# Kernel optimization log

Hardware: AMD Instinct MI355X
Metric: run time of the kernel (lower is better)

The kernel has to match this reference:

```python
import jax, jax.numpy as jnp
import numpy as np

B, N, H, STEPS, IN_DIM, OUT_DIM = 512, 81, 128, 16, 10, 9
LN_EPS = 1e-5


def _build_edges():
    # Sudoku constraint graph: edge (j -> i) if cells share row, col, or 3x3 box.
    edges = []
    for i in range(81):
        ri, ci = divmod(i, 9)
        bi = ri // 3 * 3 + ci // 3
        for j in range(81):
            if i == j:
                continue
            rj, cj = divmod(j, 9)
            bj = rj // 3 * 3 + cj // 3
            if ri == rj or ci == cj or bi == bj:
                edges.append((j, i))
    e = np.asarray(edges, dtype=np.int32).T  # [2, 1620]
    return e[0], e[1]


def setup_inputs() -> dict:
    key = jax.random.key(0)
    ks = jax.random.split(key, 24)
    s = 0.02

    def w(k, shape):
        return jax.random.normal(k, shape, dtype=jnp.float32) * s

    src_np, dst_np = _build_edges()
    inp = {
        "x": jax.random.normal(ks[0], (B, N, IN_DIM), dtype=jnp.float32),
        "src": jnp.asarray(src_np),
        "dst": jnp.asarray(dst_np),
        "W_in": w(ks[1], (IN_DIM, H)), "b_in": jnp.zeros((H,), jnp.float32),
        "pos": w(ks[2], (N, H)),
        # message MLP: (2H -> H -> H -> H -> H), ReLU between
        "mW0": w(ks[3], (2 * H, H)), "mb0": jnp.zeros((H,), jnp.float32),
        "mW1": w(ks[4], (H, H)), "mb1": jnp.zeros((H,), jnp.float32),
        "mW2": w(ks[5], (H, H)), "mb2": jnp.zeros((H,), jnp.float32),
        "mW3": w(ks[6], (H, H)), "mb3": jnp.zeros((H,), jnp.float32),
        # node MLP: (3H -> H -> H -> H -> H)
        "nW0": w(ks[7], (3 * H, H)), "nb0": jnp.zeros((H,), jnp.float32),
        "nW1": w(ks[8], (H, H)), "nb1": jnp.zeros((H,), jnp.float32),
        "nW2": w(ks[9], (H, H)), "nb2": jnp.zeros((H,), jnp.float32),
        "nW3": w(ks[10], (H, H)), "nb3": jnp.zeros((H,), jnp.float32),
        "ln_g": jnp.ones((H,), jnp.float32), "ln_b": jnp.zeros((H,), jnp.float32),
        "W_out": w(ks[11], (H, OUT_DIM)), "b_out": jnp.zeros((OUT_DIM,), jnp.float32),
    }
    return inp


def _mlp(x, Ws, bs):
    for W, b in zip(Ws[:-1], bs[:-1]):
        x = jax.nn.relu(x @ W + b)
    return x @ Ws[-1] + bs[-1]


def _layer_norm(h, g, b):
    mu = jnp.mean(h, axis=-1, keepdims=True)
    var = jnp.mean(jnp.square(h - mu), axis=-1, keepdims=True)
    return (h - mu) * jax.lax.rsqrt(var + LN_EPS) * g + b


def reference(x, src, dst, W_in, b_in, pos,
              mW0, mb0, mW1, mb1, mW2, mb2, mW3, mb3,
              nW0, nb0, nW1, nb1, nW2, nb2, nW3, nb3,
              ln_g, ln_b, W_out, b_out):
    mWs, mbs = [mW0, mW1, mW2, mW3], [mb0, mb1, mb2, mb3]
    nWs, nbs = [nW0, nW1, nW2, nW3], [nb0, nb1, nb2, nb3]

    x_embed = x @ W_in + b_in + pos  # [B, N, H]
    h = x_embed
    for _ in range(STEPS):
        h_src = h[:, src]  # [B, E, H] gather
        h_dst = h[:, dst]
        messages = _mlp(jnp.concatenate([h_src, h_dst], axis=-1), mWs, mbs)  # [B, E, H]
        # scatter-add over dst -> [B, N, H]
        aggregated = jnp.zeros_like(h).at[:, dst, :].add(messages)
        h = h + _mlp(jnp.concatenate([h, x_embed, aggregated], axis=-1), nWs, nbs)
        h = _layer_norm(h, ln_g, ln_b)
    return h @ W_out + b_out  # [B, N, 9]
```

## Files before the change

### kernel.cpp

```cpp
#include <hip/hip_runtime.h>
#include <hip/hip_bf16.h>

typedef __bf16 bf16_t;
typedef bf16_t bf16x8 __attribute__((ext_vector_type(8)));
typedef bf16_t bf16x4 __attribute__((ext_vector_type(4)));
typedef float  f32x4  __attribute__((ext_vector_type(4)));
typedef float  f32x16 __attribute__((ext_vector_type(16)));
typedef __hip_bfloat162 bf2;

#define NN   81
#define BB   512
#define BN   41472
#define EE   1620

__device__ __forceinline__ int swz(int r, int k) {
    return (r << 7) + ((((k >> 3) ^ (r & 7)) << 3) | (k & 7));
}

__device__ __forceinline__ int wpack(int n, int k) {
    return ((n >> 6) << 13) + (((((k >> 5) << 2) + ((n >> 4) & 3))) << 9)
         + (((((k >> 3) & 3) << 4) + (n & 15)) << 3) + (k & 7);
}

__device__ __forceinline__ int wpack32(int n, int k) {
    return ((((k >> 4) << 2) | (n >> 5)) << 9)
         + (((((k >> 3) & 1) << 5) | (n & 31)) << 3) + (k & 7);
}

__device__ __forceinline__ unsigned pkbf(float lo, float hi) {
    unsigned a = __float_as_uint(lo) + 0x8000u;
    unsigned b = __float_as_uint(hi) + 0x8000u;
    return __builtin_amdgcn_perm(b, a, 0x07060302);
}

__device__ __forceinline__ unsigned pkbf_t(float lo, float hi) {
    return __builtin_amdgcn_perm(__float_as_uint(hi), __float_as_uint(lo), 0x07060302);
}

__device__ __forceinline__ unsigned addrelu2(unsigned pd, unsigned qd) {
    unsigned zz = 0u;
    bf2 p = *(bf2*)&pd, q = *(bf2*)&qd, z = *(bf2*)&zz;
    bf2 r = __hmax2(__hadd2(p, q), z);
    return *(unsigned*)&r;
}

__device__ __forceinline__ void stage_act_f32(bf16_t* act, const float* __restrict__ src, int tid) {
    for (int ch = tid; ch < 2048; ch += 256) {
        int r = ch >> 4, p = ch & 15;
        const float4 a = *(const float4*)(src + (size_t)r * 128 + p * 8);
        const float4 b = *(const float4*)(src + (size_t)r * 128 + p * 8 + 4);
        uint4 o;
        o.x = pkbf(a.x, a.y); o.y = pkbf(a.z, a.w);
        o.z = pkbf(b.x, b.y); o.w = pkbf(b.z, b.w);
        *(uint4*)&act[swz(r, p << 3)] = o;
    }
}

__device__ __forceinline__ void gemm128s(f32x4 (&acc)[4][4], const bf16_t* act,
                                         const bf16_t* __restrict__ Wp,
                                         int wm, int wn, int lane, int lrow, int q) {
    f32x4 z = {0.f, 0.f, 0.f, 0.f};
    #pragma unroll
    for (int i = 0; i < 4; i++)
        #pragma unroll
        for (int j = 0; j < 4; j++) acc[i][j] = z;
    const bf16_t* wbase = Wp + (wn << 13) + (lane << 3);
    #pragma unroll
    for (int k0 = 0; k0 < 128; k0 += 32) {
        bf16x8 af[4], wf[4];
        #pragma unroll
        for (int mt = 0; mt < 4; mt++)
            af[mt] = *(const bf16x8*)&act[swz(wm * 64 + mt * 16 + lrow, k0 + q * 8)];
        #pragma unroll
        for (int nt = 0; nt < 4; nt++)
            wf[nt] = *(const bf16x8*)(wbase + ((((k0 >> 5) << 2) + nt) << 9));
        #pragma unroll
        for (int nt = 0; nt < 4; nt++)
            #pragma unroll
            for (int mt = 0; mt < 4; mt++)
                acc[nt][mt] = __builtin_amdgcn_mfma_f32_16x16x32_bf16(wf[nt], af[mt], acc[nt][mt], 0, 0, 0);
    }
}

__device__ __forceinline__ void gemm32x32(f32x16 (&acc)[2][2], const bf16_t* act,
                                          const bf16_t* __restrict__ Wp,
                                          const float* __restrict__ bias,
                                          int wm, int wn, int lane) {
    int lm = lane & 31, h = lane >> 5;
    #pragma unroll
    for (int nt = 0; nt < 2; nt++)
        #pragma unroll
        for (int g = 0; g < 4; g++) {
            float4 b4 = *(const float4*)&bias[wn * 64 + nt * 32 + 8 * g + 4 * h];
            #pragma unroll
            for (int mt = 0; mt < 2; mt++) {
                acc[nt][mt][4 * g + 0] = b4.x; acc[nt][mt][4 * g + 1] = b4.y;
                acc[nt][mt][4 * g + 2] = b4.z; acc[nt][mt][4 * g + 3] = b4.w;
            }
        }
    const bf16_t* wl = Wp + ((wn * 2) << 9) + (lane << 3);
    #pragma unroll
    for (int kk = 0; kk < 8; kk++) {
        bf16x8 af[2], wf[2];
        #pragma unroll
        for (int mt = 0; mt < 2; mt++)
            af[mt] = *(const bf16x8*)&act[swz(wm * 64 + mt * 32 + lm, kk * 16 + h * 8)];
        #pragma unroll
        for (int nt = 0; nt < 2; nt++)
            wf[nt] = *(const bf16x8*)(wl + (((kk << 2) + nt) << 9));
        #pragma unroll
        for (int nt = 0; nt < 2; nt++)
            #pragma unroll
            for (int mt = 0; mt < 2; mt++)
                acc[nt][mt] = __builtin_amdgcn_mfma_f32_32x32x16_bf16(wf[nt], af[mt], acc[nt][mt], 0, 0, 0);
    }
}

__device__ __forceinline__ void wb32x32(bf16_t* act, f32x16 (&acc)[2][2], int wm, int wn, int lane) {
    int lm = lane & 31, h = lane >> 5;
    #pragma unroll
    for (int nt = 0; nt < 2; nt++)
        #pragma unroll
        for (int g = 0; g < 4; g++) {
            int nb = wn * 64 + nt * 32 + 8 * g + 4 * h;
            #pragma unroll
            for (int mt = 0; mt < 2; mt++) {
                int m = wm * 64 + mt * 32 + lm;
                uint2 u;
                u.x = pkbf_t(fmaxf(acc[nt][mt][4 * g + 0], 0.f), fmaxf(acc[nt][mt][4 * g + 1], 0.f));
                u.y = pkbf_t(fmaxf(acc[nt][mt][4 * g + 2], 0.f), fmaxf(acc[nt][mt][4 * g + 3], 0.f));
                *(uint2*)&act[swz(m, nb)] = u;
            }
        }
}

__device__ __forceinline__ void gemm32s(f32x4 (&acc)[2][2], const bf16_t* act,
                                        const bf16_t* __restrict__ Wp,
                                        int wid, int lane, int lrow, int q, bool zero) {
    if (zero) {
        f32x4 z = {0.f, 0.f, 0.f, 0.f};
        acc[0][0] = z; acc[0][1] = z; acc[1][0] = z; acc[1][1] = z;
    }
    int wn = wid >> 1, ntb = (wid & 1) << 1;
    const bf16_t* wbase = Wp + (wn << 13) + (lane << 3);
    #pragma unroll
    for (int k0 = 0; k0 < 128; k0 += 32) {
        bf16x8 af[2], wf[2];
        af[0] = *(const bf16x8*)&act[swz(lrow, k0 + q * 8)];
        af[1] = *(const bf16x8*)&act[swz(16 + lrow, k0 + q * 8)];
        wf[0] = *(const bf16x8*)(wbase + ((((k0 >> 5) << 2) + ntb) << 9));
        wf[1] = *(const bf16x8*)(wbase + ((((k0 >> 5) << 2) + ntb + 1) << 9));
        #pragma unroll
        for (int nt = 0; nt < 2; nt++)
            #pragma unroll
            for (int mt = 0; mt < 2; mt++)
                acc[nt][mt] = __builtin_amdgcn_mfma_f32_16x16x32_bf16(wf[nt], af[mt], acc[nt][mt], 0, 0, 0);
    }
}

__device__ __forceinline__ void wb32(bf16_t* act, f32x4 (&acc)[2][2], const float* __restrict__ bias,
                                     int colb, int lrow, int q) {
    #pragma unroll
    for (int nt = 0; nt < 2; nt++) {
        int nb = colb + nt * 16 + q * 4;
        float4 b4 = *(const float4*)&bias[nb];
        #pragma unroll
        for (int mt = 0; mt < 2; mt++) {
            int m = mt * 16 + lrow;
            uint2 u;
            u.x = pkbf_t(fmaxf(acc[nt][mt][0] + b4.x, 0.f), fmaxf(acc[nt][mt][1] + b4.y, 0.f));
            u.y = pkbf_t(fmaxf(acc[nt][mt][2] + b4.z, 0.f), fmaxf(acc[nt][mt][3] + b4.w, 0.f));
            *(uint2*)&act[swz(m, nb)] = u;
        }
    }
}


__global__ __launch_bounds__(256) void k_embed(const float* __restrict__ x, const float* __restrict__ W_in,
                                               const float* __restrict__ b_in, const float* __restrict__ pos,
                                               float* __restrict__ h) {
    int idx = blockIdx.x * 256 + threadIdx.x;
    int row = idx >> 7, col = idx & 127;
    int n = row % NN;
    const float* xr = x + (size_t)row * 10;
    float s = b_in[col] + pos[n * 128 + col];
    #pragma unroll
    for (int k = 0; k < 10; k++) s += xr[k] * W_in[k * 128 + col];
    h[idx] = s;
}

struct PackArgs { const float* s[9]; };

__global__ __launch_bounds__(256) void k_pack_all(PackArgs pa, bf16_t* __restrict__ dst) {
    const int slot[9] = {0, 1, 2, 3, 4, 6, 7, 8, 9};
    int idx = blockIdx.x * 256 + threadIdx.x;
    int w = idx >> 14, r = idx & 16383;
    int n = r >> 7, k = r & 127;
    int po = (w == 2 || w == 3) ? wpack32(n, k) : wpack(n, k);
    dst[slot[w] * 16384 + po] = (bf16_t)pa.s[w][k * 128 + n];
}

__global__ __launch_bounds__(256) void k_fuse(const float* __restrict__ mW3, const float* __restrict__ nW0,
                                              bf16_t* __restrict__ Ft) {
    int idx = blockIdx.x * 256 + threadIdx.x;
    int n = idx >> 7, k = idx & 127;
    float s = 0.f;
    for (int j = 0; j < 128; j++) s += mW3[k * 128 + j] * nW0[(256 + j) * 128 + n];
    Ft[wpack(n, k)] = (bf16_t)s;
}

__global__ __launch_bounds__(128) void k_bias(const float* __restrict__ nb0, const float* __restrict__ mb3,
                                              const float* __restrict__ nW0, float* __restrict__ bfix) {
    int n = threadIdx.x;
    float s = 0.f;
    for (int j = 0; j < 128; j++) s += mb3[j] * nW0[(256 + j) * 128 + n];
    bfix[n] = nb0[n] + 20.f * s;
}

__global__ __launch_bounds__(256, 2) void k_simple3(const float* __restrict__ in,
                                                    const bf16_t* __restrict__ Wp,
                                                    const float* __restrict__ bfix,
                                                    const float* __restrict__ mb0,
                                                    float* __restrict__ C2,
                                                    bf16_t* __restrict__ Pd,
                                                    bf16_t* __restrict__ Qd) {
    __shared__ __align__(16) bf16_t act[16384];
    int tid = threadIdx.x;
    int sel = blockIdx.x / 324, blk = blockIdx.x - sel * 324;
    size_t i0 = (size_t)blk * 128;
    int lane = tid & 63, wid = tid >> 6;
    int wm = wid >> 1, wn = wid & 1, lrow = lane & 15, q = lane >> 4;

    stage_act_f32(act, in + i0 * 128, tid);
    __syncthreads();
    const bf16_t* W = Wp + (sel == 0 ? 9 * 16384 : (sel == 1 ? 0 : 16384));
    f32x4 acc[4][4];
    gemm128s(acc, act, W, wm, wn, lane, lrow, q);
    #pragma unroll
    for (int nt = 0; nt < 4; nt++) {
        int nb = wn * 64 + nt * 16 + q * 4;
        float4 b4 = (sel == 0) ? *(const float4*)&bfix[nb]
                  : (sel == 2) ? *(const float4*)&mb0[nb]
                               : make_float4(0.f, 0.f, 0.f, 0.f);
        #pragma unroll
        for (int mt = 0; mt < 4; mt++) {
            int m = wm * 64 + mt * 16 + lrow;
            float v0 = acc[nt][mt][0] + b4.x, v1 = acc[nt][mt][1] + b4.y;
            float v2 = acc[nt][mt][2] + b4.z, v3 = acc[nt][mt][3] + b4.w;
            if (sel == 0) {
                float4 o; o.x = v0; o.y = v1; o.z = v2; o.w = v3;
                *(float4*)(C2 + (i0 + m) * 128 + nb) = o;
            } else {
                uint2 u; u.x = pkbf(v0, v1); u.y = pkbf(v2, v3);
                bf16_t* dst = (sel == 1) ? Pd : Qd;
                *(uint2*)(dst + (i0 + m) * 128 + nb) = u;
            }
        }
    }
}

__global__ __launch_bounds__(256, 4) void k_edge(const bf16_t* __restrict__ P, const bf16_t* __restrict__ Q,
                                                 const int* __restrict__ src, const bf16_t* __restrict__ Wp,
                                                 const float* __restrict__ mb1, const float* __restrict__ mb2,
                                                 bf16_t* __restrict__ SA) {
    __shared__ __align__(16) bf16_t act[16384];
    int tid = threadIdx.x;
    int g = blockIdx.x, b = blockIdx.y;
    int e0 = g * 120, n0 = g * 6;
    int nreal = (e0 + 120 <= EE) ? 120 : (EE - e0);
    int lane = tid & 63, wid = tid >> 6;
    int wm = wid >> 1, wn = wid & 1;

    for (int ch = tid; ch < 2048; ch += 256) {
        int r = ch >> 4, p = ch & 15;
        uint4 o;
        if (r < nreal) {
            int e = e0 + r;
            int sn = src[e];
            int dn = n0 + r / 20;
            uint4 pv = *(const uint4*)(P + (((size_t)b * NN + sn) << 7) + (p << 3));
            uint4 qv = *(const uint4*)(Q + (((size_t)b * NN + dn) << 7) + (p << 3));
            o.x = addrelu2(pv.x, qv.x);
            o.y = addrelu2(pv.y, qv.y);
            o.z = addrelu2(pv.z, qv.z);
            o.w = addrelu2(pv.w, qv.w);
        } else {
            o.x = 0u; o.y = 0u; o.z = 0u; o.w = 0u;
        }
        *(uint4*)&act[swz(r, p << 3)] = o;
    }
    __syncthreads();

    f32x16 acc[2][2];
    gemm32x32(acc, act, Wp + 2 * 16384, mb1, wm, wn, lane);
    __syncthreads();
    wb32x32(act, acc, wm, wn, lane);
    __syncthreads();
    gemm32x32(acc, act, Wp + 3 * 16384, mb2, wm, wn, lane);
    __syncthreads();
    wb32x32(act, acc, wm, wn, lane);
    __syncthreads();

    if (tid < 192) {
        int j = tid >> 5;
        int sub = tid & 31;
        int rr = sub >> 1;
        int half = sub & 1;
        int nodes = nreal / 20;
        if (j < nodes) {
            float s0 = 0.f, s1 = 0.f, s2 = 0.f, s3 = 0.f, s4 = 0.f, s5 = 0.f, s6 = 0.f, s7 = 0.f;
            #pragma unroll
            for (int i = 0; i < 10; i++) {
                int m = 20 * j + half * 10 + i;
                bf16x8 v = *(const bf16x8*)&act[swz(m, rr << 3)];
                s0 += (float)v[0]; s1 += (float)v[1]; s2 += (float)v[2]; s3 += (float)v[3];
                s4 += (float)v[4]; s5 += (float)v[5]; s6 += (float)v[6]; s7 += (float)v[7];
            }
            s0 += __shfl_xor(s0, 1); s1 += __shfl_xor(s1, 1);
            s2 += __shfl_xor(s2, 1); s3 += __shfl_xor(s3, 1);
            s4 += __shfl_xor(s4, 1); s5 += __shfl_xor(s5, 1);
            s6 += __shfl_xor(s6, 1); s7 += __shfl_xor(s7, 1);
            if (half == 0) {
                uint4 o;
                o.x = pkbf(s0, s1); o.y = pkbf(s2, s3);
                o.z = pkbf(s4, s5); o.w = pkbf(s6, s7);
                *(uint4*)(SA + (((size_t)b * NN + n0 + j) << 7) + (rr << 3)) = o;
            }
        }
    }
}

__global__ __launch_bounds__(256, 6) void k_node(float* __restrict__ h, const bf16_t* __restrict__ SA,
                                                 const float* __restrict__ C2, const bf16_t* __restrict__ Wp,
                                                 const float* __restrict__ nb1, const float* __restrict__ nb2,
                                                 const float* __restrict__ nb3, const float* __restrict__ ln_g,
                                                 const float* __restrict__ ln_b, const float* __restrict__ mb0,
                                                 bf16_t* __restrict__ Pd, bf16_t* __restrict__ Qd) {
    __shared__ __align__(16) bf16_t act[4096];
    __shared__ __align__(16) bf16_t sab[4096];
    __shared__ float st[256];
    int tid = threadIdx.x;
    size_t i0 = (size_t)blockIdx.x * 32;
    int lane = tid & 63, wid = tid >> 6;
    int lrow = lane & 15, q = lane >> 4;
    int colb = wid * 32;

    for (int ch = tid; ch < 1024; ch += 256) {
        if (ch < 512) {
            int r = ch >> 4, p = ch & 15;
            const float4 a = *(const float4*)(h + (i0 + r) * 128 + (p << 3));
            const float4 c = *(const float4*)(h + (i0 + r) * 128 + (p << 3) + 4);
            uint4 o;
            o.x = pkbf(a.x, a.y); o.y = pkbf(a.z, a.w);
            o.z = pkbf(c.x, c.y); o.w = pkbf(c.z, c.w);
            *(uint4*)&act[swz(r, p << 3)] = o;
        } else {
            int r = (ch - 512) >> 4, p = ch & 15;
            *(uint4*)&sab[swz(r, p << 3)] = *(const uint4*)(SA + (i0 + r) * 128 + (p << 3));
        }
    }
    __syncthreads();
    f32x4 acc[2][2];
    gemm32s(acc, act, Wp + 4 * 16384, wid, lane, lrow, q, true);
    gemm32s(acc, sab, Wp + 5 * 16384, wid, lane, lrow, q, false);
    __syncthreads();
    #pragma unroll
    for (int nt = 0; nt < 2; nt++) {
        int nb = colb + nt * 16 + q * 4;
        #pragma unroll
        for (int mt = 0; mt < 2; mt++) {
            int m = mt * 16 + lrow;
            float4 c4 = *(const float4*)(C2 + (i0 + m) * 128 + nb);
            uint2 u;
            u.x = pkbf_t(fmaxf(acc[nt][mt][0] + c4.x, 0.f), fmaxf(acc[nt][mt][1] + c4.y, 0.f));
            u.y = pkbf_t(fmaxf(acc[nt][mt][2] + c4.z, 0.f), fmaxf(acc[nt][mt][3] + c4.w, 0.f));
            *(uint2*)&act[swz(m, nb)] = u;
        }
    }
    __syncthreads();
    gemm32s(acc, act, Wp + 6 * 16384, wid, lane, lrow, q, true);
    __syncthreads();
    wb32(act, acc, nb1, colb, lrow, q);
    __syncthreads();
    gemm32s(acc, act, Wp + 7 * 16384, wid, lane, lrow, q, true);
    __syncthreads();
    wb32(act, acc, nb2, colb, lrow, q);
    __syncthreads();
    gemm32s(acc, act, Wp + 8 * 16384, wid, lane, lrow, q, true);

    float s1[2] = {0.f, 0.f}, s2[2] = {0.f, 0.f};
    #pragma unroll
    for (int nt = 0; nt < 2; nt++) {
        int nb = colb + nt * 16 + q * 4;
        float4 b4 = *(const float4*)&nb3[nb];
        #pragma unroll
        for (int mt = 0; mt < 2; mt++) {
            int m = mt * 16 + lrow;
            float4 h4 = *(const float4*)(h + (i0 + m) * 128 + nb);
            float v0 = acc[nt][mt][0] + b4.x + h4.x;
            float v1 = acc[nt][mt][1] + b4.y + h4.y;
            float v2 = acc[nt][mt][2] + b4.z + h4.z;
            float v3 = acc[nt][mt][3] + b4.w + h4.w;
            acc[nt][mt][0] = v0; acc[nt][mt][1] = v1;
            acc[nt][mt][2] = v2; acc[nt][mt][3] = v3;
            s1[mt] += v0 + v1 + v2 + v3;
            s2[mt] += v0 * v0 + v1 * v1 + v2 * v2 + v3 * v3;
        }
    }
    #pragma unroll
    for (int mt = 0; mt < 2; mt++) {
        float a = s1[mt], c = s2[mt];
        a += __shfl_xor(a, 16); c += __shfl_xor(c, 16);
        a += __shfl_xor(a, 32); c += __shfl_xor(c, 32);
        s1[mt] = a; s2[mt] = c;
    }
    if (q == 0) {
        #pragma unroll
        for (int mt = 0; mt < 2; mt++) {
            st[(mt * 16 + lrow) * 8 + wid * 2 + 0] = s1[mt];
            st[(mt * 16 + lrow) * 8 + wid * 2 + 1] = s2[mt];
        }
    }
    __syncthreads();
    float mu[2], rs[2];
    #pragma unroll
    for (int mt = 0; mt < 2; mt++) {
        int m = mt * 16 + lrow;
        float a = st[m * 8 + 0] + st[m * 8 + 2] + st[m * 8 + 4] + st[m * 8 + 6];
        float c = st[m * 8 + 1] + st[m * 8 + 3] + st[m * 8 + 5] + st[m * 8 + 7];
        a *= (1.f / 128.f); c *= (1.f / 128.f);
        mu[mt] = a;
        rs[mt] = rsqrtf(c - a * a + 1e-5f);
    }
    #pragma unroll
    for (int nt = 0; nt < 2; nt++) {
        int nb = colb + nt * 16 + q * 4;
        float4 g4 = *(const float4*)&ln_g[nb];
        float4 bb4 = *(const float4*)&ln_b[nb];
        #pragma unroll
        for (int mt = 0; mt < 2; mt++) {
            int m = mt * 16 + lrow;
            float4 o4;
            o4.x = (acc[nt][mt][0] - mu[mt]) * rs[mt] * g4.x + bb4.x;
            o4.y = (acc[nt][mt][1] - mu[mt]) * rs[mt] * g4.y + bb4.y;
            o4.z = (acc[nt][mt][2] - mu[mt]) * rs[mt] * g4.z + bb4.z;
            o4.w = (acc[nt][mt][3] - mu[mt]) * rs[mt] * g4.w + bb4.w;
            *(float4*)(h + (i0 + m) * 128 + nb) = o4;
            uint2 u;
            u.x = pkbf(o4.x, o4.y); u.y = pkbf(o4.z, o4.w);
            *(uint2*)&act[swz(m, nb)] = u;
        }
    }
    __syncthreads();
    gemm32s(acc, act, Wp + 0 * 16384, wid, lane, lrow, q, true);
    #pragma unroll
    for (int nt = 0; nt < 2; nt++) {
        int nb = colb + nt * 16 + q * 4;
        #pragma unroll
        for (int mt = 0; mt < 2; mt++) {
            int m = mt * 16 + lrow;
            uint2 u;
            u.x = pkbf(acc[nt][mt][0], acc[nt][mt][1]);
            u.y = pkbf(acc[nt][mt][2], acc[nt][mt][3]);
            *(uint2*)(Pd + (i0 + m) * 128 + nb) = u;
        }
    }
    gemm32s(acc, act, Wp + 1 * 16384, wid, lane, lrow, q, true);
    #pragma unroll
    for (int nt = 0; nt < 2; nt++) {
        int nb = colb + nt * 16 + q * 4;
        float4 m4 = *(const float4*)&mb0[nb];
        #pragma unroll
        for (int mt = 0; mt < 2; mt++) {
            int m = mt * 16 + lrow;
            uint2 u;
            u.x = pkbf(acc[nt][mt][0] + m4.x, acc[nt][mt][1] + m4.y);
            u.y = pkbf(acc[nt][mt][2] + m4.z, acc[nt][mt][3] + m4.w);
            *(uint2*)(Qd + (i0 + m) * 128 + nb) = u;
        }
    }
}

__global__ __launch_bounds__(256) void k_out(const float* __restrict__ h, const float* __restrict__ W_out,
                                             const float* __restrict__ b_out, float* __restrict__ out) {
    int idx = blockIdx.x * 256 + threadIdx.x;
    int row = idx / 9, o = idx - row * 9;
    const float4* h4 = (const float4*)(h + (size_t)row * 128);
    float s = b_out[o];
    #pragma unroll 8
    for (int k4 = 0; k4 < 32; k4++) {
        float4 v = h4[k4];
        int kb = k4 * 4;
        s += v.x * W_out[kb * 9 + o] + v.y * W_out[(kb + 1) * 9 + o]
           + v.z * W_out[(kb + 2) * 9 + o] + v.w * W_out[(kb + 3) * 9 + o];
    }
    out[idx] = s;
}

extern "C" void kernel_launch(void* const* d_in, const int* in_sizes, int n_in,
                              void* d_out, int out_size, void* d_ws, size_t ws_size,
                              hipStream_t stream) {
    const float* x    = (const float*)d_in[0];
    const int*   src  = (const int*)d_in[1];
    const float* W_in = (const float*)d_in[3];
    const float* b_in = (const float*)d_in[4];
    const float* pos  = (const float*)d_in[5];
    const float* mW0  = (const float*)d_in[6];
    const float* mb0  = (const float*)d_in[7];
    const float* mW1  = (const float*)d_in[8];
    const float* mb1  = (const float*)d_in[9];
    const float* mW2  = (const float*)d_in[10];
    const float* mb2  = (const float*)d_in[11];
    const float* mW3  = (const float*)d_in[12];
    const float* mb3  = (const float*)d_in[13];
    const float* nW0  = (const float*)d_in[14];
    const float* nb0  = (const float*)d_in[15];
    const float* nW1  = (const float*)d_in[16];
    const float* nb1  = (const float*)d_in[17];
    const float* nW2  = (const float*)d_in[18];
    const float* nb2  = (const float*)d_in[19];
    const float* nW3  = (const float*)d_in[20];
    const float* nb3  = (const float*)d_in[21];
    const float* ln_g = (const float*)d_in[22];
    const float* ln_b = (const float*)d_in[23];
    const float* W_out= (const float*)d_in[24];
    const float* b_out= (const float*)d_in[25];

    char* ws = (char*)d_ws;
    float*  h   = (float*)ws;
    float*  C2  = (float*)(ws + 21233664);
    bf16_t* SA  = (bf16_t*)(ws + 42467328);
    bf16_t* P   = (bf16_t*)(ws + 53084160);
    bf16_t* Q   = (bf16_t*)(ws + 63700992);
    bf16_t* Wp  = (bf16_t*)(ws + 74317824);
    float*  bfix= (float*)(ws + 74645504);

    k_embed<<<20736, 256, 0, stream>>>(x, W_in, b_in, pos, h);

    PackArgs pa;
    pa.s[0] = mW0;  pa.s[1] = mW0 + 16384; pa.s[2] = mW1; pa.s[3] = mW2;
    pa.s[4] = nW0;  pa.s[5] = nW1;  pa.s[6] = nW2;  pa.s[7] = nW3;  pa.s[8] = nW0 + 16384;
    k_pack_all<<<576, 256, 0, stream>>>(pa, Wp);
    k_fuse<<<64, 256, 0, stream>>>(mW3, nW0, Wp + 5 * 16384);
    k_bias<<<1, 128, 0, stream>>>(nb0, mb3, nW0, bfix);

    k_simple3<<<972, 256, 0, stream>>>(h, Wp, bfix, mb0, C2, P, Q);

    for (int s = 0; s < 16; s++) {
        k_edge<<<dim3(14, 512), 256, 0, stream>>>(P, Q, src, Wp, mb1, mb2, SA);
        k_node<<<1296, 256, 0, stream>>>(h, SA, C2, Wp, nb1, nb2, nb3, ln_g, ln_b, mb0, P, Q);
    }
    k_out<<<1458, 256, 0, stream>>>(h, W_out, b_out, (float*)d_out);
}
```

Measured before the change: 2.424 ms.

## Give each wave its own 32 edge rows in k_edge, dropping block barriers

Restructures the edge kernel so each wave owns 32 edge rows across all 128 output columns. The gather of P and Q with the add-relu now feeds the first MFMA straight from registers instead of being staged through LDS. Because the two intermediate GEMM write-backs only touch the wave's own rows, the __syncthreads between layers become compiler-only fences, leaving one barrier before the reduction. In exchange each wave loads the full weight matrix instead of half, and holds a larger accumulator set, which raises register pressure.

```diff
diff --git a/kernel.cpp b/kernel.cpp
--- a/kernel.cpp
+++ b/kernel.cpp
@@ -3,7 +3,6 @@
 
 typedef __bf16 bf16_t;
 typedef bf16_t bf16x8 __attribute__((ext_vector_type(8)));
-typedef bf16_t bf16x4 __attribute__((ext_vector_type(4)));
 typedef float  f32x4  __attribute__((ext_vector_type(4)));
 typedef float  f32x16 __attribute__((ext_vector_type(16)));
 typedef __hip_bfloat162 bf2;
@@ -12,6 +11,8 @@
 #define BB   512
 #define BN   41472
 #define EE   1620
+
+#define LDS_FENCE() __asm__ volatile("" ::: "memory")
 
 __device__ __forceinline__ int swz(int r, int k) {
     return (r << 7) + ((((k >> 3) ^ (r & 7)) << 3) | (k & 7));
@@ -80,58 +81,6 @@
             for (int mt = 0; mt < 4; mt++)
                 acc[nt][mt] = __builtin_amdgcn_mfma_f32_16x16x32_bf16(wf[nt], af[mt], acc[nt][mt], 0, 0, 0);
     }
-}
-
-__device__ __forceinline__ void gemm32x32(f32x16 (&acc)[2][2], const bf16_t* act,
-                                          const bf16_t* __restrict__ Wp,
-                                          const float* __restrict__ bias,
-                                          int wm, int wn, int lane) {
-    int lm = lane & 31, h = lane >> 5;
-    #pragma unroll
-    for (int nt = 0; nt < 2; nt++)
-        #pragma unroll
-        for (int g = 0; g < 4; g++) {
-            float4 b4 = *(const float4*)&bias[wn * 64 + nt * 32 + 8 * g + 4 * h];
-            #pragma unroll
-            for (int mt = 0; mt < 2; mt++) {
-                acc[nt][mt][4 * g + 0] = b4.x; acc[nt][mt][4 * g + 1] = b4.y;
-                acc[nt][mt][4 * g + 2] = b4.z; acc[nt][mt][4 * g + 3] = b4.w;
-            }
-        }
-    const bf16_t* wl = Wp + ((wn * 2) << 9) + (lane << 3);
-    #pragma unroll
-    for (int kk = 0; kk < 8; kk++) {
-        bf16x8 af[2], wf[2];
-        #pragma unroll
-        for (int mt = 0; mt < 2; mt++)
-            af[mt] = *(const bf16x8*)&act[swz(wm * 64 + mt * 32 + lm, kk * 16 + h * 8)];
-        #pragma unroll
-        for (int nt = 0; nt < 2; nt++)
-            wf[nt] = *(const bf16x8*)(wl + (((kk << 2) + nt) << 9));
-        #pragma unroll
-        for (int nt = 0; nt < 2; nt++)
-            #pragma unroll
-            for (int mt = 0; mt < 2; mt++)
-                acc[nt][mt] = __builtin_amdgcn_mfma_f32_32x32x16_bf16(wf[nt], af[mt], acc[nt][mt], 0, 0, 0);
-    }
-}
-
-__device__ __forceinline__ void wb32x32(bf16_t* act, f32x16 (&acc)[2][2], int wm, int wn, int lane) {
-    int lm = lane & 31, h = lane >> 5;
-    #pragma unroll
-    for (int nt = 0; nt < 2; nt++)
-        #pragma unroll
-        for (int g = 0; g < 4; g++) {
-            int nb = wn * 64 + nt * 32 + 8 * g + 4 * h;
-            #pragma unroll
-            for (int mt = 0; mt < 2; mt++) {
-                int m = wm * 64 + mt * 32 + lm;
-                uint2 u;
-                u.x = pkbf_t(fmaxf(acc[nt][mt][4 * g + 0], 0.f), fmaxf(acc[nt][mt][4 * g + 1], 0.f));
-                u.y = pkbf_t(fmaxf(acc[nt][mt][4 * g + 2], 0.f), fmaxf(acc[nt][mt][4 * g + 3], 0.f));
-                *(uint2*)&act[swz(m, nb)] = u;
-            }
-        }
 }
 
 __device__ __forceinline__ void gemm32s(f32x4 (&acc)[2][2], const bf16_t* act,
@@ -268,37 +217,87 @@
     int g = blockIdx.x, b = blockIdx.y;
     int e0 = g * 120, n0 = g * 6;
     int nreal = (e0 + 120 <= EE) ? 120 : (EE - e0);
-    int lane = tid & 63, wid = tid >> 6;
-    int wm = wid >> 1, wn = wid & 1;
-
-    for (int ch = tid; ch < 2048; ch += 256) {
-        int r = ch >> 4, p = ch & 15;
-        uint4 o;
-        if (r < nreal) {
-            int e = e0 + r;
-            int sn = src[e];
-            int dn = n0 + r / 20;
-            uint4 pv = *(const uint4*)(P + (((size_t)b * NN + sn) << 7) + (p << 3));
-            uint4 qv = *(const uint4*)(Q + (((size_t)b * NN + dn) << 7) + (p << 3));
-            o.x = addrelu2(pv.x, qv.x);
-            o.y = addrelu2(pv.y, qv.y);
-            o.z = addrelu2(pv.z, qv.z);
-            o.w = addrelu2(pv.w, qv.w);
+    int lane = tid & 63, w = tid >> 6;
+    int lm = lane & 31, h = lane >> 5;
+    int r = (w << 5) + lm;
+    bool rok = (r < nreal);
+    int rr0 = rok ? r : 0;
+    int sn = src[e0 + rr0];
+    int dn = n0 + rr0 / 20;
+    const bf16_t* prow = P + (((size_t)b * NN + sn) << 7) + (h << 3);
+    const bf16_t* qrow = Q + (((size_t)b * NN + dn) << 7) + (h << 3);
+
+    f32x16 acc[4];
+    #pragma unroll
+    for (int nt = 0; nt < 4; nt++)
+        #pragma unroll
+        for (int g4 = 0; g4 < 4; g4++) {
+            float4 b4 = *(const float4*)&mb1[nt * 32 + 8 * g4 + 4 * h];
+            acc[nt][4 * g4 + 0] = b4.x; acc[nt][4 * g4 + 1] = b4.y;
+            acc[nt][4 * g4 + 2] = b4.z; acc[nt][4 * g4 + 3] = b4.w;
+        }
+    const bf16_t* wl1 = Wp + 2 * 16384 + (lane << 3);
+    #pragma unroll
+    for (int kk = 0; kk < 8; kk++) {
+        bf16x8 af;
+        if (rok) {
+            uint4 pv = *(const uint4*)(prow + kk * 16);
+            uint4 qv = *(const uint4*)(qrow + kk * 16);
+            uint4 o;
+            o.x = addrelu2(pv.x, qv.x); o.y = addrelu2(pv.y, qv.y);
+            o.z = addrelu2(pv.z, qv.z); o.w = addrelu2(pv.w, qv.w);
+            af = *(bf16x8*)&o;
         } else {
-            o.x = 0u; o.y = 0u; o.z = 0u; o.w = 0u;
-        }
-        *(uint4*)&act[swz(r, p << 3)] = o;
-    }
-    __syncthreads();
-
-    f32x16 acc[2][2];
-    gemm32x32(acc, act, Wp + 2 * 16384, mb1, wm, wn, lane);
-    __syncthreads();
-    wb32x32(act, acc, wm, wn, lane);
-    __syncthreads();
-    gemm32x32(acc, act, Wp + 3 * 16384, mb2, wm, wn, lane);
-    __syncthreads();
-    wb32x32(act, acc, wm, wn, lane);
+            #pragma unroll
+            for (int t = 0; t < 8; t++) af[t] = (bf16_t)0.f;
+        }
+        #pragma unroll
+        for (int nt = 0; nt < 4; nt++) {
+            bf16x8 wf = *(const bf16x8*)(wl1 + (((kk << 2) + nt) << 9));
+            acc[nt] = __builtin_amdgcn_mfma_f32_32x32x16_bf16(wf, af, acc[nt], 0, 0, 0);
+        }
+    }
+    #pragma unroll
+    for (int nt = 0; nt < 4; nt++)
+        #pragma unroll
+        for (int g4 = 0; g4 < 4; g4++) {
+            int n = nt * 32 + 8 * g4 + 4 * h;
+            uint2 u;
+            u.x = pkbf_t(fmaxf(acc[nt][4 * g4 + 0], 0.f), fmaxf(acc[nt][4 * g4 + 1], 0.f));
+            u.y = pkbf_t(fmaxf(acc[nt][4 * g4 + 2], 0.f), fmaxf(acc[nt][4 * g4 + 3], 0.f));
+            *(uint2*)&act[swz(r, n)] = u;
+        }
+    LDS_FENCE();
+
+    #pragma unroll
+    for (int nt = 0; nt < 4; nt++)
+        #pragma unroll
+        for (int g4 = 0; g4 < 4; g4++) {
+            float4 b4 = *(const float4*)&mb2[nt * 32 + 8 * g4 + 4 * h];
+            acc[nt][4 * g4 + 0] = b4.x; acc[nt][4 * g4 + 1] = b4.y;
+            acc[nt][4 * g4 + 2] = b4.z; acc[nt][4 * g4 + 3] = b4.w;
+        }
+    const bf16_t* wl2 = Wp + 3 * 16384 + (lane << 3);
+    #pragma unroll
+    for (int kk = 0; kk < 8; kk++) {
+        bf16x8 af = *(const bf16x8*)&act[swz(r, kk * 16 + h * 8)];
+        #pragma unroll
+        for (int nt = 0; nt < 4; nt++) {
+            bf16x8 wf = *(const bf16x8*)(wl2 + (((kk << 2) + nt) << 9));
+            acc[nt] = __builtin_amdgcn_mfma_f32_32x32x16_bf16(wf, af, acc[nt], 0, 0, 0);
+        }
+    }
+    LDS_FENCE();
+    #pragma unroll
+    for (int nt = 0; nt < 4; nt++)
+        #pragma unroll
+        for (int g4 = 0; g4 < 4; g4++) {
+            int n = nt * 32 + 8 * g4 + 4 * h;
+            uint2 u;
+            u.x = pkbf_t(fmaxf(acc[nt][4 * g4 + 0], 0.f), fmaxf(acc[nt][4 * g4 + 1], 0.f));
+            u.y = pkbf_t(fmaxf(acc[nt][4 * g4 + 2], 0.f), fmaxf(acc[nt][4 * g4 + 3], 0.f));
+            *(uint2*)&act[swz(r, n)] = u;
+        }
     __syncthreads();
 
     if (tid < 192) {
```

Result: slower. 2.693 ms (+11.1%).
